# Optimization experiments

Hardware: AMD Instinct MI355X
Metric: run time of the kernel (lower is better)

The kernel has to match this reference:

```python
import jax, jax.numpy as jnp
import numpy as np

B, C, H, W = 2048, 32, 12, 12
N = H * W          # 144, fixed by pos_embed / relative_pos in GCNBlock
K = 9              # k-NN neighbors; dilation = 1


def _sincos_1d(d, pos):
    # standard 1D sin-cos embedding (ViG get_1d_sincos_pos_embed_from_grid)
    omega = np.arange(d // 2, dtype=np.float32) / (d / 2.0)
    omega = 1.0 / 10000 ** omega
    out = np.einsum('m,d->md', pos.astype(np.float32), omega)
    return np.concatenate([np.sin(out), np.cos(out)], axis=1)


def _relative_pos_table(dim, grid_size):
    # ViG get_2d_relative_pos_embed; Grapher stores the NEGATED table as a
    # frozen buffer that is ADDED to the pairwise distances before top-k.
    gw, gh = np.meshgrid(np.arange(grid_size, dtype=np.float32),
                         np.arange(grid_size, dtype=np.float32))
    pe = np.concatenate([_sincos_1d(dim // 2, gw.reshape(-1)),
                         _sincos_1d(dim // 2, gh.reshape(-1))], axis=1)  # (N, dim)
    rel = 2.0 * pe @ pe.T / pe.shape[1]
    return (-rel[None]).astype(np.float32)  # (1, N, N); n == HW so no interpolation


def setup_inputs() -> dict:
    key = jax.random.key(0)
    ks = jax.random.split(key, 8)
    def w(k, o, i):  # kaiming-normal per model_init
        return jax.random.normal(k, (o, i), jnp.float32) * (2.0 / i) ** 0.5
    z = lambda n: jnp.zeros((n,), jnp.float32)  # biases zeroed per model_init
    return {
        'inputs': jax.random.normal(ks[0], (B, C, H, W), jnp.float32),
        'pos_embed': jax.random.normal(ks[1], (1, C, H, W), jnp.float32) * 0.02,
        'relative_pos': jnp.asarray(_relative_pos_table(C, H)),
        'g_fc1_w': w(ks[2], C, C),       'g_fc1_b': z(C),
        'g_conv_w': w(ks[3], 2 * C, 2 * C), 'g_conv_b': z(2 * C),
        'g_fc2_w': w(ks[4], C, 2 * C),   'g_fc2_b': z(C),
        'f_fc1_w': w(ks[5], C, C),       'f_fc1_b': z(C),
        'f_fc2_w': w(ks[6], C, C),       'f_fc2_b': z(C),
    }


def _conv1x1(x, w, b):  # x: (B, Cin, H, W), w: (Cout, Cin)
    return jnp.einsum('bchw,oc->bohw', x, w) + b[None, :, None, None]


def _forward(inputs, pos_embed, relative_pos,
             g_fc1_w, g_fc1_b, g_conv_w, g_conv_b, g_fc2_w, g_fc2_b,
             f_fc1_w, f_fc1_b, f_fc2_w, f_fc2_b):
    x = inputs + pos_embed
    # ---- Grapher_noBN ----
    tmp = x
    x1 = _conv1x1(x, g_fc1_w, g_fc1_b)
    b, c, h, w = x1.shape
    n = h * w
    xf = x1.reshape(b, c, n)  # (B, C, N) node features
    # dynamic k-NN graph (torch does this under no_grad; indices kill grads anyway)
    xn = xf / jnp.clip(jnp.linalg.norm(xf, axis=1, keepdims=True), 1e-12)
    xt = jnp.swapaxes(xn, 1, 2)                      # (B, N, C)
    sq = jnp.sum(xt * xt, axis=-1)                   # (B, N)
    dist = sq[:, :, None] - 2.0 * jnp.einsum('bnc,bmc->bnm', xt, xt) + sq[:, None, :]
    dist = dist + relative_pos                       # (B, N, N)
    _, idx = jax.lax.top_k(-dist, K)                 # (B, N, K) nearest neighbors
    # MRConv2d: max-relative aggregation
    x_j = jax.vmap(lambda f, i: f[:, i])(xf, idx)    # (B, C, N, K) gather neighbors
    m = jnp.max(x_j - xf[:, :, :, None], axis=-1)    # (B, C, N)
    # interleave [x, max_rel] along channels: (B,C,2,N) -> (B,2C,N,1)
    stacked = jnp.stack([xf, m], axis=2).reshape(b, 2 * c, n, 1)
    hc = jnp.einsum('bcnk,oc->bonk', stacked, g_conv_w) + g_conv_b[None, :, None, None]
    hc = jax.nn.gelu(hc, approximate=False)          # BasicConv act (nn.GELU)
    hc = hc.reshape(b, 2 * c, h, w)
    x = _conv1x1(hc, g_fc2_w, g_fc2_b)
    x = x + tmp                                      # DropPath = identity (eval)
    # ---- FFN ----
    sc = x
    x = _conv1x1(x, f_fc1_w, f_fc1_b)
    x = jax.nn.gelu(x, approximate=False)
    x = _conv1x1(x, f_fc2_w, f_fc2_b)
    return x + sc


def reference(inputs, pos_embed, relative_pos,
              g_fc1_w, g_fc1_b, g_conv_w, g_conv_b, g_fc2_w, g_fc2_b,
              f_fc1_w, f_fc1_b, f_fc2_w, f_fc2_b):
    return _forward(inputs, pos_embed, relative_pos,
                    g_fc1_w, g_fc1_b, g_conv_w, g_conv_b, g_fc2_w, g_fc2_b,
                    f_fc1_w, f_fc1_b, f_fc2_w, f_fc2_b)
```

## Files before the change

### kernel.cpp

```cpp
#include <hip/hip_runtime.h>
#include <math.h>

#define BATCH 2048
#define CH    32
#define NN    144
#define KNN   9
#define PAD   36

__device__ __forceinline__ float gelu_exact(float x) {
    return 0.5f * x * (1.0f + erff(x * 0.70710678118654752440f));
}

__global__ __launch_bounds__(256, 3) void gcn_main(
        const float* __restrict__ xin,
        const float* __restrict__ pos,
        const float* __restrict__ rel,
        const float* __restrict__ W1,  const float* __restrict__ B1,
        const float* __restrict__ WC,  const float* __restrict__ BC,
        const float* __restrict__ W2,  const float* __restrict__ B2,
        const float* __restrict__ F1,  const float* __restrict__ FB1,
        const float* __restrict__ F2,  const float* __restrict__ FB2,
        float* __restrict__ out) {
    const int b = blockIdx.x;
    const int t = threadIdx.x;

    __shared__ __align__(16) float s_tmpT[NN * PAD];
    __shared__ __align__(16) float s_xfT[NN * PAD];
    __shared__ __align__(16) float s_W1p[CH * PAD];
    __shared__ float s_sq[NN];
    __shared__ float s_rinv[NN];

    {
        const float4* x4 = (const float4*)(xin + (size_t)b * (CH * NN));
        const float4* p4 = (const float4*)pos;
        for (int i = t; i < (CH * NN) / 4; i += 256) {
            float4 a = x4[i], p = p4[i];
            int idx = 4 * i;
            int c = idx / NN, n = idx - c * NN;
            float* dst = &s_tmpT[n * PAD + c];
            dst[0]       = a.x + p.x;
            dst[PAD]     = a.y + p.y;
            dst[2 * PAD] = a.z + p.z;
            dst[3 * PAD] = a.w + p.w;
        }
        if (t < 256) {
            int c = t >> 3, q = t & 7;
            ((float4*)&s_W1p[c * PAD])[q] = ((const float4*)W1)[t];
        }
    }
    __syncthreads();

    {
        const int c = t & 31, n0 = t >> 5;
        float w[CH];
        const float4* wr = (const float4*)&s_W1p[c * PAD];
        #pragma unroll
        for (int q = 0; q < 8; ++q) {
            float4 v = wr[q];
            w[4*q] = v.x; w[4*q+1] = v.y; w[4*q+2] = v.z; w[4*q+3] = v.w;
        }
        const float bias = B1[c];
        #pragma unroll
        for (int r = 0; r < 18; ++r) {
            int n = n0 + 8 * r;
            const float4* row = (const float4*)&s_tmpT[n * PAD];
            float acc = bias;
            #pragma unroll
            for (int q = 0; q < 8; ++q) {
                float4 v = row[q];
                acc += w[4*q] * v.x + w[4*q+1] * v.y + w[4*q+2] * v.z + w[4*q+3] * v.w;
            }
            s_xfT[n * PAD + c] = acc;
        }
    }
    __syncthreads();

    if (t < NN) {
        const float4* row = (const float4*)&s_xfT[t * PAD];
        float sum = 0.f;
        #pragma unroll
        for (int q = 0; q < 8; ++q) {
            float4 v = row[q];
            sum += v.x * v.x + v.y * v.y + v.z * v.z + v.w * v.w;
        }
        float r = 1.0f / fmaxf(sqrtf(sum), 1e-12f);
        s_rinv[t] = r;
        s_sq[t]   = sum * r * r;
    }
    __syncthreads();

    if (t >= NN) return;
    const int n = t;

    float xnc[CH];
    {
        const float rr = s_rinv[n];
        const float4* row = (const float4*)&s_xfT[n * PAD];
        #pragma unroll
        for (int q = 0; q < 8; ++q) {
            float4 v = row[q];
            xnc[4*q] = v.x * rr; xnc[4*q+1] = v.y * rr;
            xnc[4*q+2] = v.z * rr; xnc[4*q+3] = v.w * rr;
        }
    }
    const float sqn = s_sq[n];
    float bestd[KNN];
    int   besti[KNN];
    #pragma unroll
    for (int k = 0; k < KNN; ++k) { bestd[k] = INFINITY; besti[k] = 0; }

    const float* reln = rel + n * NN;
    for (int mb = 0; mb < NN / 16; ++mb) {
        float rl[16];
        const float4* rp = (const float4*)(reln + mb * 16);
        #pragma unroll
        for (int q = 0; q < 4; ++q) {
            float4 v = rp[q];
            rl[4*q] = v.x; rl[4*q+1] = v.y; rl[4*q+2] = v.z; rl[4*q+3] = v.w;
        }
        #pragma unroll
        for (int mm = 0; mm < 16; ++mm) {
            const int m = mb * 16 + mm;
            const float4* row = (const float4*)&s_xfT[m * PAD];
            float dot = 0.f;
            #pragma unroll
            for (int q = 0; q < 8; ++q) {
                float4 v = row[q];
                dot += xnc[4*q] * v.x + xnc[4*q+1] * v.y
                     + xnc[4*q+2] * v.z + xnc[4*q+3] * v.w;
            }
            float d = sqn - 2.0f * (dot * s_rinv[m]) + s_sq[m] + rl[mm];
            if (d < bestd[KNN - 1]) {
                bestd[KNN - 1] = d; besti[KNN - 1] = m;
                #pragma unroll
                for (int k = KNN - 1; k > 0; --k) {
                    if (bestd[k] < bestd[k - 1]) {
                        float td = bestd[k]; bestd[k] = bestd[k - 1]; bestd[k - 1] = td;
                        int   ti = besti[k]; besti[k] = besti[k - 1]; besti[k - 1] = ti;
                    }
                }
            }
        }
    }

    float stc[2 * CH];
    {
        const float4* row = (const float4*)&s_xfT[n * PAD];
        #pragma unroll
        for (int q = 0; q < 8; ++q) {
            float4 v = row[q];
            stc[8*q + 0] = v.x; stc[8*q + 2] = v.y;
            stc[8*q + 4] = v.z; stc[8*q + 6] = v.w;
        }
        #pragma unroll
        for (int c = 0; c < CH; ++c) stc[2*c + 1] = -INFINITY;
        #pragma unroll
        for (int k = 0; k < KNN; ++k) {
            const float4* nr = (const float4*)&s_xfT[besti[k] * PAD];
            #pragma unroll
            for (int q = 0; q < 8; ++q) {
                float4 v = nr[q];
                stc[8*q + 1] = fmaxf(stc[8*q + 1], v.x);
                stc[8*q + 3] = fmaxf(stc[8*q + 3], v.y);
                stc[8*q + 5] = fmaxf(stc[8*q + 5], v.z);
                stc[8*q + 7] = fmaxf(stc[8*q + 7], v.w);
            }
        }
        #pragma unroll
        for (int c = 0; c < CH; ++c) stc[2*c + 1] -= stc[2*c];
    }

    float x2r[CH];
    {
        const float4* trow = (const float4*)&s_tmpT[n * PAD];
        #pragma unroll
        for (int q = 0; q < 8; ++q) {
            float4 v = trow[q];
            x2r[4*q]   = B2[4*q]   + v.x;
            x2r[4*q+1] = B2[4*q+1] + v.y;
            x2r[4*q+2] = B2[4*q+2] + v.z;
            x2r[4*q+3] = B2[4*q+3] + v.w;
        }
    }
    #pragma unroll 4
    for (int j = 0; j < 2 * CH; ++j) {
        float acc = BC[j];
        #pragma unroll
        for (int c = 0; c < 2 * CH; ++c) acc += WC[j * 2 * CH + c] * stc[c];
        float h = gelu_exact(acc);
        #pragma unroll
        for (int o = 0; o < CH; ++o) x2r[o] += W2[o * 2 * CH + j] * h;
    }

    float yv[CH];
    #pragma unroll
    for (int o = 0; o < CH; ++o) {
        float acc = FB1[o];
        #pragma unroll
        for (int c = 0; c < CH; ++c) acc += F1[o * CH + c] * x2r[c];
        yv[o] = gelu_exact(acc);
    }
    float* ob = out + (size_t)b * (CH * NN) + n;
    #pragma unroll
    for (int o = 0; o < CH; ++o) {
        float acc = FB2[o];
        #pragma unroll
        for (int c = 0; c < CH; ++c) acc += F2[o * CH + c] * yv[c];
        ob[o * NN] = acc + x2r[o];
    }
}

extern "C" void kernel_launch(void* const* d_in, const int* in_sizes, int n_in,
                              void* d_out, int out_size, void* d_ws, size_t ws_size,
                              hipStream_t stream) {
    const float* xin = (const float*)d_in[0];
    const float* pos = (const float*)d_in[1];
    const float* rel = (const float*)d_in[2];
    const float* w1  = (const float*)d_in[3];
    const float* b1  = (const float*)d_in[4];
    const float* wc  = (const float*)d_in[5];
    const float* bc  = (const float*)d_in[6];
    const float* w2  = (const float*)d_in[7];
    const float* b2  = (const float*)d_in[8];
    const float* f1  = (const float*)d_in[9];
    const float* fb1 = (const float*)d_in[10];
    const float* f2  = (const float*)d_in[11];
    const float* fb2 = (const float*)d_in[12];
    float* out = (float*)d_out;

    dim3 grid(BATCH), blk(256);
    gcn_main<<<grid, blk, 0, stream>>>(xin, pos, rel,
                                       w1, b1, wc, bc, w2, b2,
                                       f1, fb1, f2, fb2, out);
}
```

Before: 565.0 us.

## Process two batch samples per block with per-thread fc1 and fused norms

```diff
diff --git a/kernel.cpp b/kernel.cpp
--- a/kernel.cpp
+++ b/kernel.cpp
@@ -6,12 +6,13 @@
 #define NN    144
 #define KNN   9
 #define PAD   36
+#define ACT   (2*NN)
 
 __device__ __forceinline__ float gelu_exact(float x) {
     return 0.5f * x * (1.0f + erff(x * 0.70710678118654752440f));
 }
 
-__global__ __launch_bounds__(256, 3) void gcn_main(
+__global__ __launch_bounds__(320) void gcn_main(
         const float* __restrict__ xin,
         const float* __restrict__ pos,
         const float* __restrict__ rel,
@@ -21,89 +22,44 @@
         const float* __restrict__ F1,  const float* __restrict__ FB1,
         const float* __restrict__ F2,  const float* __restrict__ FB2,
         float* __restrict__ out) {
-    const int b = blockIdx.x;
     const int t = threadIdx.x;
+    const int g = (t >= NN) ? 1 : 0;
+    const int n = t - g * NN;
+    const long bb = (long)blockIdx.x * 2 + g;
 
-    __shared__ __align__(16) float s_tmpT[NN * PAD];
-    __shared__ __align__(16) float s_xfT[NN * PAD];
-    __shared__ __align__(16) float s_W1p[CH * PAD];
-    __shared__ float s_sq[NN];
-    __shared__ float s_rinv[NN];
+    __shared__ __align__(16) float  s_xfT[2][NN * PAD];
+    __shared__ float2 s_sr[2][NN];
 
-    {
-        const float4* x4 = (const float4*)(xin + (size_t)b * (CH * NN));
-        const float4* p4 = (const float4*)pos;
-        for (int i = t; i < (CH * NN) / 4; i += 256) {
-            float4 a = x4[i], p = p4[i];
-            int idx = 4 * i;
-            int c = idx / NN, n = idx - c * NN;
-            float* dst = &s_tmpT[n * PAD + c];
-            dst[0]       = a.x + p.x;
-            dst[PAD]     = a.y + p.y;
-            dst[2 * PAD] = a.z + p.z;
-            dst[3 * PAD] = a.w + p.w;
+    const float* xb = xin + bb * (CH * NN) + n;
+    const float* pb = pos + n;
+
+    float xf_n[CH];
+
+    if (t < ACT) {
+        float tc[CH];
+        #pragma unroll
+        for (int c = 0; c < CH; ++c) tc[c] = xb[c * NN] + pb[c * NN];
+        float sum = 0.f;
+        #pragma unroll
+        for (int o = 0; o < CH; ++o) {
+            float acc = B1[o];
+            #pragma unroll
+            for (int c = 0; c < CH; ++c) acc += W1[o * CH + c] * tc[c];
+            xf_n[o] = acc;
+            sum += acc * acc;
         }
-        if (t < 256) {
-            int c = t >> 3, q = t & 7;
-            ((float4*)&s_W1p[c * PAD])[q] = ((const float4*)W1)[t];
-        }
+        float4* xr = (float4*)&s_xfT[g][n * PAD];
+        #pragma unroll
+        for (int q = 0; q < 8; ++q)
+            xr[q] = make_float4(xf_n[4*q], xf_n[4*q+1], xf_n[4*q+2], xf_n[4*q+3]);
+        float r = 1.0f / fmaxf(sqrtf(sum), 1e-12f);
+        s_sr[g][n] = make_float2(sum * r * r, r);
     }
     __syncthreads();
+    if (t >= ACT) return;
 
-    {
-        const int c = t & 31, n0 = t >> 5;
-        float w[CH];
-        const float4* wr = (const float4*)&s_W1p[c * PAD];
-        #pragma unroll
-        for (int q = 0; q < 8; ++q) {
-            float4 v = wr[q];
-            w[4*q] = v.x; w[4*q+1] = v.y; w[4*q+2] = v.z; w[4*q+3] = v.w;
-        }
-        const float bias = B1[c];
-        #pragma unroll
-        for (int r = 0; r < 18; ++r) {
-            int n = n0 + 8 * r;
-            const float4* row = (const float4*)&s_tmpT[n * PAD];
-            float acc = bias;
-            #pragma unroll
-            for (int q = 0; q < 8; ++q) {
-                float4 v = row[q];
-                acc += w[4*q] * v.x + w[4*q+1] * v.y + w[4*q+2] * v.z + w[4*q+3] * v.w;
-            }
-            s_xfT[n * PAD + c] = acc;
-        }
-    }
-    __syncthreads();
-
-    if (t < NN) {
-        const float4* row = (const float4*)&s_xfT[t * PAD];
-        float sum = 0.f;
-        #pragma unroll
-        for (int q = 0; q < 8; ++q) {
-            float4 v = row[q];
-            sum += v.x * v.x + v.y * v.y + v.z * v.z + v.w * v.w;
-        }
-        float r = 1.0f / fmaxf(sqrtf(sum), 1e-12f);
-        s_rinv[t] = r;
-        s_sq[t]   = sum * r * r;
-    }
-    __syncthreads();
-
-    if (t >= NN) return;
-    const int n = t;
-
-    float xnc[CH];
-    {
-        const float rr = s_rinv[n];
-        const float4* row = (const float4*)&s_xfT[n * PAD];
-        #pragma unroll
-        for (int q = 0; q < 8; ++q) {
-            float4 v = row[q];
-            xnc[4*q] = v.x * rr; xnc[4*q+1] = v.y * rr;
-            xnc[4*q+2] = v.z * rr; xnc[4*q+3] = v.w * rr;
-        }
-    }
-    const float sqn = s_sq[n];
+    const float rn  = s_sr[g][n].y;
+    const float sqn = s_sr[g][n].x;
     float bestd[KNN];
     int   besti[KNN];
     #pragma unroll
@@ -121,15 +77,16 @@
         #pragma unroll
         for (int mm = 0; mm < 16; ++mm) {
             const int m = mb * 16 + mm;
-            const float4* row = (const float4*)&s_xfT[m * PAD];
+            const float4* row = (const float4*)&s_xfT[g][m * PAD];
             float dot = 0.f;
             #pragma unroll
             for (int q = 0; q < 8; ++q) {
                 float4 v = row[q];
-                dot += xnc[4*q] * v.x + xnc[4*q+1] * v.y
-                     + xnc[4*q+2] * v.z + xnc[4*q+3] * v.w;
+                dot += xf_n[4*q] * v.x + xf_n[4*q+1] * v.y
+                     + xf_n[4*q+2] * v.z + xf_n[4*q+3] * v.w;
             }
-            float d = sqn - 2.0f * (dot * s_rinv[m]) + s_sq[m] + rl[mm];
+            float2 sr = s_sr[g][m];
+            float d = sqn - 2.0f * (dot * (rn * sr.y)) + sr.x + rl[mm];
             if (d < bestd[KNN - 1]) {
                 bestd[KNN - 1] = d; besti[KNN - 1] = m;
                 #pragma unroll
@@ -143,50 +100,35 @@
         }
     }
 
-    float stc[2 * CH];
-    {
-        const float4* row = (const float4*)&s_xfT[n * PAD];
+    float x2r[CH];
+    #pragma unroll
+    for (int o = 0; o < CH; ++o) x2r[o] = B2[o] + xb[o * NN] + pb[o * NN];
+
+    float mrel[CH];
+    #pragma unroll
+    for (int c = 0; c < CH; ++c) mrel[c] = -INFINITY;
+    #pragma unroll
+    for (int k = 0; k < KNN; ++k) {
+        const float4* nr = (const float4*)&s_xfT[g][besti[k] * PAD];
         #pragma unroll
         for (int q = 0; q < 8; ++q) {
-            float4 v = row[q];
-            stc[8*q + 0] = v.x; stc[8*q + 2] = v.y;
-            stc[8*q + 4] = v.z; stc[8*q + 6] = v.w;
-        }
-        #pragma unroll
-        for (int c = 0; c < CH; ++c) stc[2*c + 1] = -INFINITY;
-        #pragma unroll
-        for (int k = 0; k < KNN; ++k) {
-            const float4* nr = (const float4*)&s_xfT[besti[k] * PAD];
-            #pragma unroll
-            for (int q = 0; q < 8; ++q) {
-                float4 v = nr[q];
-                stc[8*q + 1] = fmaxf(stc[8*q + 1], v.x);
-                stc[8*q + 3] = fmaxf(stc[8*q + 3], v.y);
-                stc[8*q + 5] = fmaxf(stc[8*q + 5], v.z);
-                stc[8*q + 7] = fmaxf(stc[8*q + 7], v.w);
-            }
-        }
-        #pragma unroll
-        for (int c = 0; c < CH; ++c) stc[2*c + 1] -= stc[2*c];
-    }
-
-    float x2r[CH];
-    {
-        const float4* trow = (const float4*)&s_tmpT[n * PAD];
-        #pragma unroll
-        for (int q = 0; q < 8; ++q) {
-            float4 v = trow[q];
-            x2r[4*q]   = B2[4*q]   + v.x;
-            x2r[4*q+1] = B2[4*q+1] + v.y;
-            x2r[4*q+2] = B2[4*q+2] + v.z;
-            x2r[4*q+3] = B2[4*q+3] + v.w;
+            float4 v = nr[q];
+            mrel[4*q]   = fmaxf(mrel[4*q],   v.x);
+            mrel[4*q+1] = fmaxf(mrel[4*q+1], v.y);
+            mrel[4*q+2] = fmaxf(mrel[4*q+2], v.z);
+            mrel[4*q+3] = fmaxf(mrel[4*q+3], v.w);
         }
     }
-    #pragma unroll 4
+    #pragma unroll
+    for (int c = 0; c < CH; ++c) mrel[c] -= xf_n[c];
+
+    #pragma unroll 2
     for (int j = 0; j < 2 * CH; ++j) {
         float acc = BC[j];
+        const float* wr = WC + j * 2 * CH;
         #pragma unroll
-        for (int c = 0; c < 2 * CH; ++c) acc += WC[j * 2 * CH + c] * stc[c];
+        for (int c = 0; c < CH; ++c)
+            acc += wr[2*c] * xf_n[c] + wr[2*c + 1] * mrel[c];
         float h = gelu_exact(acc);
         #pragma unroll
         for (int o = 0; o < CH; ++o) x2r[o] += W2[o * 2 * CH + j] * h;
@@ -200,7 +142,7 @@
         for (int c = 0; c < CH; ++c) acc += F1[o * CH + c] * x2r[c];
         yv[o] = gelu_exact(acc);
     }
-    float* ob = out + (size_t)b * (CH * NN) + n;
+    float* ob = out + bb * (CH * NN) + n;
     #pragma unroll
     for (int o = 0; o < CH; ++o) {
         float acc = FB2[o];
@@ -228,7 +170,7 @@
     const float* fb2 = (const float*)d_in[12];
     float* out = (float*)d_out;
 
-    dim3 grid(BATCH), blk(256);
+    dim3 grid(BATCH / 2), blk(320);
     gcn_main<<<grid, blk, 0, stream>>>(xin, pos, rel,
                                        w1, b1, wc, bc, w2, b2,
                                        f1, fb1, f2, fb2, out);
```

Result: slower. 650.6 us (+15.1%).
